# Optimization experiments

Measured on AMD Instinct MI355X. Metric: run time of the kernel, lower is better.

The kernel has to match this reference:

```python
import jax, jax.numpy as jnp
import numpy as np

N = 100000
E = 1600000
F_IN = 512
HID = 8
HEADS = 8
NCLS = 16
NEG_SLOPE = 0.2
EPS = 1e-16


def gat_conv(x, W, att_src, att_dst, bias, src, dst, heads, ch, concat):
    n = x.shape[0]
    xl = (x @ W).reshape(n, heads, ch)              # [N,H,C]
    a_src = (xl * att_src).sum(-1)                  # [N,H]
    a_dst = (xl * att_dst).sum(-1)                  # [N,H]
    alpha = jax.nn.leaky_relu(a_src[src] + a_dst[dst], NEG_SLOPE)  # [E,H]
    amax = jax.ops.segment_max(alpha, dst, num_segments=n)         # [N,H]
    ex = jnp.exp(alpha - amax[dst])                                 # [E,H]
    denom = jax.ops.segment_sum(ex, dst, num_segments=n)           # [N,H]
    coef = ex / (denom[dst] + EPS)                                  # [E,H]
    msg = xl[src] * coef[:, :, None]                                # [E,H,C]
    out = jax.ops.segment_sum(msg, dst, num_segments=n)            # [N,H,C]
    out = out.reshape(n, heads * ch) if concat else out.mean(axis=1)
    return out + bias


def setup_inputs() -> dict:
    key = jax.random.key(0)
    ks = jax.random.split(key, 12)
    x = jax.random.normal(ks[0], (N, F_IN), dtype=jnp.float32)
    edge_index = jax.random.randint(ks[1], (2, E), 0, N, dtype=jnp.int32)
    s1 = 1.0 / np.sqrt(F_IN)
    s2 = 1.0 / np.sqrt(HID * HEADS)
    return {
        "x": x,
        "edge_index": edge_index,
        "W1": jax.random.normal(ks[2], (F_IN, HEADS * HID), dtype=jnp.float32) * s1,
        "att_src1": jax.random.normal(ks[3], (HEADS, HID), dtype=jnp.float32),
        "att_dst1": jax.random.normal(ks[4], (HEADS, HID), dtype=jnp.float32),
        "bias1": jnp.zeros((HEADS * HID,), dtype=jnp.float32),
        "W2": jax.random.normal(ks[5], (HEADS * HID, NCLS), dtype=jnp.float32) * s2,
        "att_src2": jax.random.normal(ks[6], (1, NCLS), dtype=jnp.float32),
        "att_dst2": jax.random.normal(ks[7], (1, NCLS), dtype=jnp.float32),
        "bias2": jnp.zeros((NCLS,), dtype=jnp.float32),
    }


def reference(x, edge_index, W1, att_src1, att_dst1, bias1, W2, att_src2, att_dst2, bias2):
    src, dst = edge_index[0], edge_index[1]
    # eval mode: all dropout layers are identity
    h = gat_conv(x, W1, att_src1, att_dst1, bias1, src, dst, HEADS, HID, True)
    h = jax.nn.elu(h)
    out = gat_conv(h, W2, att_src2, att_dst2, bias2, src, dst, 1, NCLS, False)
    return out
```

## Files before the change

### kernel.cpp

```cpp
#include <hip/hip_runtime.h>
#include <math.h>

#define N_NODES 100000
#define N_EDGES 1600000
#define F_IN    512
#define HID     8
#define HEADS   8
#define NCLS    16
#define NEG_SLOPE 0.2f
#define EPS_F   1e-16f
#define DEG_CAP 64
#define G1_BLOCKS 782
#define CSR_EPB 1024
#define CSR_BLOCKS 1563

__device__ __forceinline__ float lrelu(float a) {
    return a >= 0.f ? a : NEG_SLOPE * a;
}

__global__ __launch_bounds__(256) void fused1_kernel(
    const float* __restrict__ x, const float* __restrict__ W1,
    const float* __restrict__ att_src, const float* __restrict__ att_dst,
    float* __restrict__ xl1, float* __restrict__ a_src1, float* __restrict__ a_dst1,
    const int* __restrict__ src, const int* __restrict__ dst,
    int* __restrict__ cnt, int* __restrict__ csr_src) {
    __shared__ float xs[128][33];
    __shared__ float wsh[32][68];
    const int tid = threadIdx.x;

    if (blockIdx.x >= G1_BLOCKS) {
        int e0 = (blockIdx.x - G1_BLOCKS) * CSR_EPB + tid;
        int d[4], s[4];
        bool v[4];
#pragma unroll
        for (int q = 0; q < 4; q++) {
            int e = e0 + q * 256;
            v[q] = e < N_EDGES;
            if (v[q]) { d[q] = dst[e]; s[q] = src[e]; }
        }
        int pos[4];
#pragma unroll
        for (int q = 0; q < 4; q++)
            if (v[q]) pos[q] = atomicAdd(&cnt[d[q]], 1);
#pragma unroll
        for (int q = 0; q < 4; q++)
            if (v[q] && pos[q] < DEG_CAP)
                csr_src[(size_t)d[q] * DEG_CAP + pos[q]] = s[q];
        return;
    }

    const int nb  = blockIdx.x * 128;
    const int ng  = tid >> 3;
    const int cg  = tid & 7;

    float acc[4][8];
#pragma unroll
    for (int i = 0; i < 4; i++)
#pragma unroll
        for (int j = 0; j < 8; j++) acc[i][j] = 0.f;

    for (int kb = 0; kb < F_IN; kb += 32) {
#pragma unroll
        for (int q = 0; q < 4; q++) {
            int idx = tid + q * 256;
            int nl  = idx >> 3;
            int kq  = (idx & 7) * 4;
            int node = nb + nl; if (node >= N_NODES) node = N_NODES - 1;
            float4 vv = *(const float4*)&x[(size_t)node * F_IN + kb + kq];
            xs[nl][kq + 0] = vv.x; xs[nl][kq + 1] = vv.y;
            xs[nl][kq + 2] = vv.z; xs[nl][kq + 3] = vv.w;
        }
#pragma unroll
        for (int q = 0; q < 2; q++) {
            int idx = tid + q * 256;
            int kk  = idx >> 4;
            int cq  = (idx & 15) * 4;
            *(float4*)&wsh[kk][cq] = *(const float4*)&W1[(size_t)(kb + kk) * 64 + cq];
        }
        __syncthreads();
#pragma unroll
        for (int kk = 0; kk < 32; kk++) {
            float xa0 = xs[ng * 4 + 0][kk];
            float xa1 = xs[ng * 4 + 1][kk];
            float xa2 = xs[ng * 4 + 2][kk];
            float xa3 = xs[ng * 4 + 3][kk];
            float4 w0 = *(const float4*)&wsh[kk][cg * 8];
            float4 w1 = *(const float4*)&wsh[kk][cg * 8 + 4];
            float wa[8] = {w0.x, w0.y, w0.z, w0.w, w1.x, w1.y, w1.z, w1.w};
#pragma unroll
            for (int j = 0; j < 8; j++) {
                acc[0][j] += xa0 * wa[j];
                acc[1][j] += xa1 * wa[j];
                acc[2][j] += xa2 * wa[j];
                acc[3][j] += xa3 * wa[j];
            }
        }
        __syncthreads();
    }
    float4 s0 = *(const float4*)&att_src[cg * 8];
    float4 s1 = *(const float4*)&att_src[cg * 8 + 4];
    float4 d0 = *(const float4*)&att_dst[cg * 8];
    float4 d1 = *(const float4*)&att_dst[cg * 8 + 4];
    float sv[8] = {s0.x, s0.y, s0.z, s0.w, s1.x, s1.y, s1.z, s1.w};
    float dv[8] = {d0.x, d0.y, d0.z, d0.w, d1.x, d1.y, d1.z, d1.w};
#pragma unroll
    for (int i = 0; i < 4; i++) {
        int node = nb + ng * 4 + i;
        if (node < N_NODES) {
            *(float4*)&xl1[(size_t)node * 64 + cg * 8] =
                make_float4(acc[i][0], acc[i][1], acc[i][2], acc[i][3]);
            *(float4*)&xl1[(size_t)node * 64 + cg * 8 + 4] =
                make_float4(acc[i][4], acc[i][5], acc[i][6], acc[i][7]);
            float as = 0.f, ad = 0.f;
#pragma unroll
            for (int j = 0; j < 8; j++) { as += acc[i][j] * sv[j]; ad += acc[i][j] * dv[j]; }
            a_src1[node * 8 + cg] = as;
            a_dst1[node * 8 + cg] = ad;
        }
    }
}

__global__ __launch_bounds__(256) void aggr1_kernel(
    const int* __restrict__ cnt, const int* __restrict__ csr_src,
    const float* __restrict__ a_src1, const float* __restrict__ a_dst1,
    const float* __restrict__ xl1, float* __restrict__ agg1) {
    int n = (blockIdx.x * 256 + threadIdx.x) >> 6;
    int lane = threadIdx.x & 63;
    if (n >= N_NODES) return;
    int h = lane >> 3;
    const int* bucket = &csr_src[(size_t)n * DEG_CAP];
    int c = cnt[n]; c = c < DEG_CAP ? c : DEG_CAP;
    float ad = a_dst1[n * 8 + h];
    float m = -INFINITY, l = 0.f, acc = 0.f;
    int i = 0;
    for (; i + 8 <= c; i += 8) {
        int s[8];
#pragma unroll
        for (int q = 0; q < 8; q++) s[q] = bucket[i + q];
        float al[8], xv[8];
#pragma unroll
        for (int q = 0; q < 8; q++) al[q] = lrelu(a_src1[s[q] * 8 + h] + ad);
#pragma unroll
        for (int q = 0; q < 8; q++) xv[q] = xl1[(size_t)s[q] * 64 + lane];
        float nm = m;
#pragma unroll
        for (int q = 0; q < 8; q++) nm = fmaxf(nm, al[q]);
        float scale = __expf(m - nm);
        float le = 0.f, ae = 0.f;
#pragma unroll
        for (int q = 0; q < 8; q++) {
            float e = __expf(al[q] - nm);
            le += e;
            ae += e * xv[q];
        }
        l = l * scale + le;
        acc = acc * scale + ae;
        m = nm;
    }
    for (; i < c; i++) {
        int s = bucket[i];
        float alpha = lrelu(a_src1[s * 8 + h] + ad);
        float nm = fmaxf(m, alpha);
        float scale = __expf(m - nm);
        float e1 = __expf(alpha - nm);
        float xv = xl1[(size_t)s * 64 + lane];
        l = l * scale + e1;
        acc = acc * scale + e1 * xv;
        m = nm;
    }
    agg1[(size_t)n * 64 + lane] = acc / (l + EPS_F);
}

__global__ __launch_bounds__(256) void node2_kernel(
    const float* __restrict__ agg1, const float* __restrict__ bias1,
    const float* __restrict__ W2,
    const float* __restrict__ att_src2, const float* __restrict__ att_dst2,
    float* __restrict__ xl2, float* __restrict__ a_src2, float* __restrict__ a_dst2) {
    int i = blockIdx.x * 256 + threadIdx.x;
    int n = i >> 4, j = i & 15;
    float acc = 0.f;
#pragma unroll
    for (int ii = 0; ii < 16; ii++) {
        float4 a4 = *(const float4*)&agg1[(size_t)n * 64 + ii * 4];
        float4 b4 = *(const float4*)&bias1[ii * 4];
        float v0 = a4.x + b4.x; v0 = v0 > 0.f ? v0 : (__expf(v0) - 1.f);
        float v1 = a4.y + b4.y; v1 = v1 > 0.f ? v1 : (__expf(v1) - 1.f);
        float v2 = a4.z + b4.z; v2 = v2 > 0.f ? v2 : (__expf(v2) - 1.f);
        float v3 = a4.w + b4.w; v3 = v3 > 0.f ? v3 : (__expf(v3) - 1.f);
        acc += v0 * W2[(ii * 4 + 0) * 16 + j] + v1 * W2[(ii * 4 + 1) * 16 + j]
             + v2 * W2[(ii * 4 + 2) * 16 + j] + v3 * W2[(ii * 4 + 3) * 16 + j];
    }
    xl2[i] = acc;
    float s = acc * att_src2[j];
    float d = acc * att_dst2[j];
#pragma unroll
    for (int m = 8; m >= 1; m >>= 1) {
        s += __shfl_xor(s, m, 16);
        d += __shfl_xor(d, m, 16);
    }
    if (j == 0) {
        a_src2[n] = s; a_dst2[n] = d;
    }
}

__global__ __launch_bounds__(256) void aggr2_kernel(
    const int* __restrict__ cnt, const int* __restrict__ csr_src,
    const float* __restrict__ a_src2, const float* __restrict__ a_dst2,
    const float* __restrict__ xl2, const float* __restrict__ bias2,
    float* __restrict__ out) {
    int idx = blockIdx.x * 256 + threadIdx.x;
    int n = idx >> 4;
    int j = idx & 15;
    if (n >= N_NODES) return;
    const int* bucket = &csr_src[(size_t)n * DEG_CAP];
    int c = cnt[n]; c = c < DEG_CAP ? c : DEG_CAP;
    float ad = a_dst2[n];
    float m = -INFINITY, l = 0.f, acc = 0.f;
    int i = 0;
    for (; i + 4 <= c; i += 4) {
        int s0 = bucket[i + 0];
        int s1 = bucket[i + 1];
        int s2 = bucket[i + 2];
        int s3 = bucket[i + 3];
        float al0 = lrelu(a_src2[s0] + ad);
        float al1 = lrelu(a_src2[s1] + ad);
        float al2 = lrelu(a_src2[s2] + ad);
        float al3 = lrelu(a_src2[s3] + ad);
        float xv0 = xl2[(size_t)s0 * 16 + j];
        float xv1 = xl2[(size_t)s1 * 16 + j];
        float xv2 = xl2[(size_t)s2 * 16 + j];
        float xv3 = xl2[(size_t)s3 * 16 + j];
        float nm = fmaxf(fmaxf(fmaxf(fmaxf(m, al0), al1), al2), al3);
        float scale = __expf(m - nm);
        float e0 = __expf(al0 - nm), e1 = __expf(al1 - nm);
        float e2 = __expf(al2 - nm), e3 = __expf(al3 - nm);
        l = l * scale + ((e0 + e1) + (e2 + e3));
        acc = acc * scale + ((e0 * xv0 + e1 * xv1) + (e2 * xv2 + e3 * xv3));
        m = nm;
    }
    for (; i < c; i++) {
        int s = bucket[i];
        float alpha = lrelu(a_src2[s] + ad);
        float nm = fmaxf(m, alpha);
        float scale = __expf(m - nm);
        float e1 = __expf(alpha - nm);
        float xv = xl2[(size_t)s * 16 + j];
        l = l * scale + e1;
        acc = acc * scale + e1 * xv;
        m = nm;
    }
    out[(size_t)n * 16 + j] = acc / (l + EPS_F) + bias2[j];
}

extern "C" void kernel_launch(void* const* d_in, const int* in_sizes, int n_in,
                              void* d_out, int out_size, void* d_ws, size_t ws_size,
                              hipStream_t stream) {
    const float* x        = (const float*)d_in[0];
    const int*   ei       = (const int*)d_in[1];
    const float* W1       = (const float*)d_in[2];
    const float* att_src1 = (const float*)d_in[3];
    const float* att_dst1 = (const float*)d_in[4];
    const float* bias1    = (const float*)d_in[5];
    const float* W2       = (const float*)d_in[6];
    const float* att_src2 = (const float*)d_in[7];
    const float* att_dst2 = (const float*)d_in[8];
    const float* bias2    = (const float*)d_in[9];
    float* out = (float*)d_out;

    const int* src = ei;
    const int* dst = ei + N_EDGES;

    float* ws = (float*)d_ws;
    float* xl1    = ws;
    float* a_src1 = xl1 + (size_t)N_NODES * 64;
    float* a_dst1 = a_src1 + (size_t)N_NODES * 8;
    float* agg1   = a_dst1 + (size_t)N_NODES * 8;
    float* xl2    = agg1 + (size_t)N_NODES * 64;
    float* a_src2 = xl2 + (size_t)N_NODES * 16;
    float* a_dst2 = a_src2 + N_NODES;
    int*   cnt    = (int*)(a_dst2 + N_NODES);
    int*   csr_src= cnt + N_NODES;

    hipMemsetAsync(cnt, 0, (size_t)N_NODES * sizeof(int), stream);

    fused1_kernel<<<G1_BLOCKS + CSR_BLOCKS, 256, 0, stream>>>(
        x, W1, att_src1, att_dst1, xl1, a_src1, a_dst1,
        src, dst, cnt, csr_src);

    aggr1_kernel<<<(N_NODES * 64 + 255) / 256, 256, 0, stream>>>(
        cnt, csr_src, a_src1, a_dst1, xl1, agg1);

    node2_kernel<<<(N_NODES * 16 + 255) / 256, 256, 0, stream>>>(
        agg1, bias1, W2, att_src2, att_dst2, xl2, a_src2, a_dst2);
    aggr2_kernel<<<(N_NODES * 16 + 255) / 256, 256, 0, stream>>>(
        cnt, csr_src, a_src2, a_dst2, xl2, bias2, out);
}
```

Before: 507.5 us.

## Store layer-1 features in bf16 and fuse node2 projection into aggr1

Layer-1 projected features are now written as bf16, halving the bytes read by the random-gather aggregation. The node2 kernel (ELU plus W2 projection and attention dot products) is folded into the end of aggr1, using shared-memory W2 and a per-wave buffer. This removes the agg1 round-trip through global memory and one kernel launch. The cost is reduced precision in the gathered features, plus a block-level sync and shared-memory staging in aggr1.

Measured after the change: 497.2 us. 2.0% less time.

```diff
diff --git a/kernel.cpp b/kernel.cpp
--- a/kernel.cpp
+++ b/kernel.cpp
@@ -17,11 +17,20 @@
 __device__ __forceinline__ float lrelu(float a) {
     return a >= 0.f ? a : NEG_SLOPE * a;
 }
+__device__ __forceinline__ unsigned short f2bf_rne(float f) {
+    unsigned b = __float_as_uint(f);
+    b += 0x7FFFu + ((b >> 16) & 1u);
+    return (unsigned short)(b >> 16);
+}
+__device__ __forceinline__ float bf2f(unsigned short u) {
+    return __uint_as_float(((unsigned)u) << 16);
+}
 
 __global__ __launch_bounds__(256) void fused1_kernel(
     const float* __restrict__ x, const float* __restrict__ W1,
     const float* __restrict__ att_src, const float* __restrict__ att_dst,
-    float* __restrict__ xl1, float* __restrict__ a_src1, float* __restrict__ a_dst1,
+    unsigned short* __restrict__ xl1b,
+    float* __restrict__ a_src1, float* __restrict__ a_dst1,
     const int* __restrict__ src, const int* __restrict__ dst,
     int* __restrict__ cnt, int* __restrict__ csr_src) {
     __shared__ float xs[128][33];
@@ -107,10 +116,13 @@
     for (int i = 0; i < 4; i++) {
         int node = nb + ng * 4 + i;
         if (node < N_NODES) {
-            *(float4*)&xl1[(size_t)node * 64 + cg * 8] =
-                make_float4(acc[i][0], acc[i][1], acc[i][2], acc[i][3]);
-            *(float4*)&xl1[(size_t)node * 64 + cg * 8 + 4] =
-                make_float4(acc[i][4], acc[i][5], acc[i][6], acc[i][7]);
+            unsigned pk[4];
+#pragma unroll
+            for (int j = 0; j < 4; j++)
+                pk[j] = (unsigned)f2bf_rne(acc[i][2 * j]) |
+                        ((unsigned)f2bf_rne(acc[i][2 * j + 1]) << 16);
+            *(uint4*)&xl1b[(size_t)node * 64 + cg * 8] =
+                make_uint4(pk[0], pk[1], pk[2], pk[3]);
             float as = 0.f, ad = 0.f;
 #pragma unroll
             for (int j = 0; j < 8; j++) { as += acc[i][j] * sv[j]; ad += acc[i][j] * dv[j]; }
@@ -123,10 +135,26 @@
 __global__ __launch_bounds__(256) void aggr1_kernel(
     const int* __restrict__ cnt, const int* __restrict__ csr_src,
     const float* __restrict__ a_src1, const float* __restrict__ a_dst1,
-    const float* __restrict__ xl1, float* __restrict__ agg1) {
-    int n = (blockIdx.x * 256 + threadIdx.x) >> 6;
-    int lane = threadIdx.x & 63;
-    if (n >= N_NODES) return;
+    const unsigned short* __restrict__ xl1b,
+    const float* __restrict__ bias1, const float* __restrict__ W2,
+    const float* __restrict__ att_src2, const float* __restrict__ att_dst2,
+    float* __restrict__ xl2, float* __restrict__ a_src2, float* __restrict__ a_dst2) {
+    __shared__ float w2s[64][17];
+    __shared__ float b1s[64];
+    __shared__ float hbuf[4][64];
+    const int tid = threadIdx.x;
+    const int w = tid >> 6;
+    const int lane = tid & 63;
+
+#pragma unroll
+    for (int q = 0; q < 4; q++) {
+        int idx = tid * 4 + q;
+        w2s[idx >> 4][idx & 15] = W2[idx];
+    }
+    if (tid < 64) b1s[tid] = bias1[tid];
+    __syncthreads();
+
+    int n = (blockIdx.x << 2) + w;
     int h = lane >> 3;
     const int* bucket = &csr_src[(size_t)n * DEG_CAP];
     int c = cnt[n]; c = c < DEG_CAP ? c : DEG_CAP;
@@ -141,7 +169,7 @@
 #pragma unroll
         for (int q = 0; q < 8; q++) al[q] = lrelu(a_src1[s[q] * 8 + h] + ad);
 #pragma unroll
-        for (int q = 0; q < 8; q++) xv[q] = xl1[(size_t)s[q] * 64 + lane];
+        for (int q = 0; q < 8; q++) xv[q] = bf2f(xl1b[(size_t)s[q] * 64 + lane]);
         float nm = m;
 #pragma unroll
         for (int q = 0; q < 8; q++) nm = fmaxf(nm, al[q]);
@@ -163,44 +191,36 @@
         float nm = fmaxf(m, alpha);
         float scale = __expf(m - nm);
         float e1 = __expf(alpha - nm);
-        float xv = xl1[(size_t)s * 64 + lane];
+        float xv = bf2f(xl1b[(size_t)s * 64 + lane]);
         l = l * scale + e1;
         acc = acc * scale + e1 * xv;
         m = nm;
     }
-    agg1[(size_t)n * 64 + lane] = acc / (l + EPS_F);
-}
-
-__global__ __launch_bounds__(256) void node2_kernel(
-    const float* __restrict__ agg1, const float* __restrict__ bias1,
-    const float* __restrict__ W2,
-    const float* __restrict__ att_src2, const float* __restrict__ att_dst2,
-    float* __restrict__ xl2, float* __restrict__ a_src2, float* __restrict__ a_dst2) {
-    int i = blockIdx.x * 256 + threadIdx.x;
-    int n = i >> 4, j = i & 15;
-    float acc = 0.f;
-#pragma unroll
-    for (int ii = 0; ii < 16; ii++) {
-        float4 a4 = *(const float4*)&agg1[(size_t)n * 64 + ii * 4];
-        float4 b4 = *(const float4*)&bias1[ii * 4];
-        float v0 = a4.x + b4.x; v0 = v0 > 0.f ? v0 : (__expf(v0) - 1.f);
-        float v1 = a4.y + b4.y; v1 = v1 > 0.f ? v1 : (__expf(v1) - 1.f);
-        float v2 = a4.z + b4.z; v2 = v2 > 0.f ? v2 : (__expf(v2) - 1.f);
-        float v3 = a4.w + b4.w; v3 = v3 > 0.f ? v3 : (__expf(v3) - 1.f);
-        acc += v0 * W2[(ii * 4 + 0) * 16 + j] + v1 * W2[(ii * 4 + 1) * 16 + j]
-             + v2 * W2[(ii * 4 + 2) * 16 + j] + v3 * W2[(ii * 4 + 3) * 16 + j];
-    }
-    xl2[i] = acc;
-    float s = acc * att_src2[j];
-    float d = acc * att_dst2[j];
-#pragma unroll
-    for (int m = 8; m >= 1; m >>= 1) {
-        s += __shfl_xor(s, m, 16);
-        d += __shfl_xor(d, m, 16);
-    }
-    if (j == 0) {
-        a_src2[n] = s; a_dst2[n] = d;
-    }
+    float agg = acc / (l + EPS_F);
+    float hv = agg + b1s[lane];
+    hv = hv > 0.f ? hv : (__expf(hv) - 1.f);
+    hbuf[w][lane] = hv;
+    __syncthreads();
+
+    const int q4 = lane >> 4;
+    const int j  = lane & 15;
+    float p = 0.f;
+#pragma unroll
+    for (int i2 = 0; i2 < 16; i2++) {
+        int k = (q4 << 4) + i2;
+        p += hbuf[w][k] * w2s[k][j];
+    }
+    p += __shfl_xor(p, 16);
+    p += __shfl_xor(p, 32);
+    float ss = p * att_src2[j];
+    float dd = p * att_dst2[j];
+#pragma unroll
+    for (int mm = 8; mm >= 1; mm >>= 1) {
+        ss += __shfl_xor(ss, mm);
+        dd += __shfl_xor(dd, mm);
+    }
+    if (lane == 0) { a_src2[n] = ss; a_dst2[n] = dd; }
+    if (lane < 16) xl2[(size_t)n * 16 + lane] = p;
 }
 
 __global__ __launch_bounds__(256) void aggr2_kernel(
@@ -271,27 +291,25 @@
     const int* dst = ei + N_EDGES;
 
     float* ws = (float*)d_ws;
-    float* xl1    = ws;
-    float* a_src1 = xl1 + (size_t)N_NODES * 64;
+    float* a_src1 = ws;
     float* a_dst1 = a_src1 + (size_t)N_NODES * 8;
-    float* agg1   = a_dst1 + (size_t)N_NODES * 8;
-    float* xl2    = agg1 + (size_t)N_NODES * 64;
+    float* xl2    = a_dst1 + (size_t)N_NODES * 8;
     float* a_src2 = xl2 + (size_t)N_NODES * 16;
     float* a_dst2 = a_src2 + N_NODES;
     int*   cnt    = (int*)(a_dst2 + N_NODES);
     int*   csr_src= cnt + N_NODES;
+    unsigned short* xl1b = (unsigned short*)(csr_src + (size_t)N_NODES * DEG_CAP);
 
     hipMemsetAsync(cnt, 0, (size_t)N_NODES * sizeof(int), stream);
 
     fused1_kernel<<<G1_BLOCKS + CSR_BLOCKS, 256, 0, stream>>>(
-        x, W1, att_src1, att_dst1, xl1, a_src1, a_dst1,
+        x, W1, att_src1, att_dst1, xl1b, a_src1, a_dst1,
         src, dst, cnt, csr_src);
 
-    aggr1_kernel<<<(N_NODES * 64 + 255) / 256, 256, 0, stream>>>(
-        cnt, csr_src, a_src1, a_dst1, xl1, agg1);
-
-    node2_kernel<<<(N_NODES * 16 + 255) / 256, 256, 0, stream>>>(
-        agg1, bias1, W2, att_src2, att_dst2, xl2, a_src2, a_dst2);
+    aggr1_kernel<<<N_NODES / 4, 256, 0, stream>>>(
+        cnt, csr_src, a_src1, a_dst1, xl1b, bias1, W2, att_src2, att_dst2,
+        xl2, a_src2, a_dst2);
+
     aggr2_kernel<<<(N_NODES * 16 + 255) / 256, 256, 0, stream>>>(
         cnt, csr_src, a_src2, a_dst2, xl2, bias2, out);
 }
```
